# Kernel tuning notes

Measured on AMD Instinct MI355X. Metric: run time of the kernel, lower is better.

## Reference

```python
import jax, jax.numpy as jnp
import numpy as np

EPS = 1e-5  # torch LayerNorm default


def setup_inputs() -> dict:
    key = jax.random.key(0)
    ks = jax.random.split(key, 16)
    B, S, E = 2, 2048, 1024
    H, DK, DV = 16, 64, 64
    s_in = 1.0 / np.sqrt(E)
    s_ctx = 1.0 / np.sqrt(H * DV)
    return {
        "Q": jax.random.normal(ks[0], (B, S, E), jnp.float32),
        "K": jax.random.normal(ks[1], (B, S, E), jnp.float32),
        "V": jax.random.normal(ks[2], (B, S, E), jnp.float32),
        "attn_mask": jax.random.randint(ks[3], (B, S, S), 0, 2).astype(bool),
        "Wq": jax.random.normal(ks[4], (E, H * DK), jnp.float32) * s_in,
        "bq": jnp.zeros((H * DK,), jnp.float32),
        "Wk": jax.random.normal(ks[5], (E, H * DK), jnp.float32) * s_in,
        "bk": jnp.zeros((H * DK,), jnp.float32),
        "Wv": jax.random.normal(ks[6], (E, H * DV), jnp.float32) * s_in,
        "bv": jnp.zeros((H * DV,), jnp.float32),
        "Wo": jax.random.normal(ks[7], (H * DV, E), jnp.float32) * s_ctx,
        "bo": jnp.zeros((E,), jnp.float32),
        "gamma": jnp.ones((E,), jnp.float32),
        "beta": jnp.zeros((E,), jnp.float32),
        "n_heads": 16,
        "d_k": 64,
        "d_v": 64,
    }


def reference(Q, K, V, attn_mask, Wq, bq, Wk, bk, Wv, bv, Wo, bo, gamma, beta,
              n_heads, d_k, d_v):
    B, S, E = Q.shape
    # QKV projections -> [B, H, S, d]
    q = (Q @ Wq + bq).reshape(B, S, n_heads, d_k).transpose(0, 2, 1, 3)
    k = (K @ Wk + bk).reshape(B, S, n_heads, d_k).transpose(0, 2, 1, 3)
    v = (V @ Wv + bv).reshape(B, S, n_heads, d_v).transpose(0, 2, 1, 3)
    # scaled dot-product attention with explicit [B,H,S,S] scores
    scores = jnp.einsum('bhqd,bhkd->bhqk', q, k) / np.sqrt(d_k).astype(jnp.float32)
    scores = jnp.where(attn_mask[:, None, :, :], jnp.float32(-1e9), scores)
    attn = jax.nn.softmax(scores, axis=-1)
    context = jnp.einsum('bhqk,bhkd->bhqd', attn, v)
    context = context.transpose(0, 2, 1, 3).reshape(B, S, n_heads * d_v)
    output = context @ Wo + bo
    # residual + LayerNorm over last dim
    x = output + Q
    mu = jnp.mean(x, axis=-1, keepdims=True)
    var = jnp.mean(jnp.square(x - mu), axis=-1, keepdims=True)
    y = (x - mu) * jax.lax.rsqrt(var + EPS) * gamma + beta
    return (y, attn)
```

## Files before the change

### kernel.cpp

```cpp
#include <hip/hip_runtime.h>
#include <cstdint>
#include <cstddef>

#define Bc 2
#define Sc 2048
#define Ec 1024
#define Hc 16
#define Dc 64
#define BSc 4096
#define BHc 32

typedef __attribute__((ext_vector_type(8))) short bf16x8;
typedef __attribute__((ext_vector_type(4))) float f32x4;

__device__ __forceinline__ uint16_t f2b(float x) {
  union { float f; uint32_t u; } v; v.f = x;
  return (uint16_t)((v.u + 0x7FFFu + ((v.u >> 16) & 1u)) >> 16);
}

__global__ void conv_bf16(const float* __restrict__ src, uint16_t* __restrict__ dst, int n) {
  int i = (blockIdx.x * blockDim.x + threadIdx.x) * 4;
  if (i < n) {
    float4 v = *(const float4*)(src + i);
    ushort4 o;
    o.x = f2b(v.x); o.y = f2b(v.y); o.z = f2b(v.z); o.w = f2b(v.w);
    *(ushort4*)(dst + i) = o;
  }
}

__global__ void transpose_bf16(const float* __restrict__ src, uint16_t* __restrict__ dst) {
  __shared__ uint16_t tile[32][33];
  int x0 = blockIdx.x * 32, y0 = blockIdx.y * 32;
  int tx = threadIdx.x & 31, ty = threadIdx.x >> 5;
#pragma unroll
  for (int i = 0; i < 32; i += 8)
    tile[ty + i][tx] = f2b(src[(size_t)(y0 + ty + i) * 1024 + x0 + tx]);
  __syncthreads();
#pragma unroll
  for (int i = 0; i < 32; i += 8)
    dst[(size_t)(x0 + ty + i) * 1024 + y0 + tx] = tile[tx][ty + i];
}

__global__ __launch_bounds__(256) void gemm_proj(
    const uint16_t* __restrict__ A, const uint16_t* __restrict__ BT,
    const float* __restrict__ bias, uint16_t* __restrict__ out, int mode) {
  const int K = 1024;
  __shared__ uint16_t As[128 * 40];
  __shared__ uint16_t Bs[128 * 40];
  int n0 = blockIdx.x * 128, m0 = blockIdx.y * 128;
  int t = threadIdx.x;
  int wave = t >> 6, lane = t & 63;
  int wm = (wave >> 1) * 64, wn = (wave & 1) * 64;
  int quad = lane >> 4, l16 = lane & 15;

  f32x4 acc[4][4];
#pragma unroll
  for (int i = 0; i < 4; i++)
#pragma unroll
    for (int j = 0; j < 4; j++) acc[i][j] = (f32x4)(0.0f);

  int srow = t >> 1, scol = (t & 1) * 16;

  for (int k0 = 0; k0 < K; k0 += 32) {
    const uint16_t* ag = A + (size_t)(m0 + srow) * K + k0 + scol;
    const uint16_t* bg = BT + (size_t)(n0 + srow) * K + k0 + scol;
    uint4 av0 = *(const uint4*)ag;
    uint4 av1 = *(const uint4*)(ag + 8);
    uint4 bv0 = *(const uint4*)bg;
    uint4 bv1 = *(const uint4*)(bg + 8);
    __syncthreads();
    *(uint4*)(As + srow * 40 + scol) = av0;
    *(uint4*)(As + srow * 40 + scol + 8) = av1;
    *(uint4*)(Bs + srow * 40 + scol) = bv0;
    *(uint4*)(Bs + srow * 40 + scol + 8) = bv1;
    __syncthreads();
    bf16x8 af[4], bfr[4];
#pragma unroll
    for (int i = 0; i < 4; i++)
      af[i] = *(const bf16x8*)(As + (wm + i * 16 + l16) * 40 + quad * 8);
#pragma unroll
    for (int j = 0; j < 4; j++)
      bfr[j] = *(const bf16x8*)(Bs + (wn + j * 16 + l16) * 40 + quad * 8);
#pragma unroll
    for (int i = 0; i < 4; i++)
#pragma unroll
      for (int j = 0; j < 4; j++)
        acc[i][j] = __builtin_amdgcn_mfma_f32_16x16x32_bf16(af[i], bfr[j], acc[i][j], 0, 0, 0);
  }
#pragma unroll
  for (int i = 0; i < 4; i++)
#pragma unroll
    for (int j = 0; j < 4; j++) {
      int col = n0 + wn + j * 16 + l16;
      float bval = bias[col];
      int h = col >> 6, d = col & 63;
#pragma unroll
      for (int r = 0; r < 4; r++) {
        int row = m0 + wm + i * 16 + quad * 4 + r;
        int b = row >> 11, s = row & 2047;
        uint16_t hv = f2b(acc[i][j][r] + bval);
        if (mode == 0)
          out[(size_t)((b * Hc + h) * Sc + s) * Dc + d] = hv;
        else
          out[(size_t)((b * Hc + h) * Dc + d) * Sc + s] = hv;
      }
    }
}

__global__ __launch_bounds__(256) void gemm_out(
    const uint16_t* __restrict__ A, const uint16_t* __restrict__ BT,
    const float* __restrict__ bias, const float* __restrict__ resid,
    float* __restrict__ x) {
  const int K = 1024;
  __shared__ uint16_t As[128 * 40];
  __shared__ uint16_t Bs[128 * 40];
  int n0 = blockIdx.x * 128, m0 = blockIdx.y * 128;
  int t = threadIdx.x;
  int wave = t >> 6, lane = t & 63;
  int wm = (wave >> 1) * 64, wn = (wave & 1) * 64;
  int quad = lane >> 4, l16 = lane & 15;

  f32x4 acc[4][4];
#pragma unroll
  for (int i = 0; i < 4; i++)
#pragma unroll
    for (int j = 0; j < 4; j++) acc[i][j] = (f32x4)(0.0f);

  int srow = t >> 1, scol = (t & 1) * 16;
  for (int k0 = 0; k0 < K; k0 += 32) {
    const uint16_t* ag = A + (size_t)(m0 + srow) * K + k0 + scol;
    const uint16_t* bg = BT + (size_t)(n0 + srow) * K + k0 + scol;
    uint4 av0 = *(const uint4*)ag;
    uint4 av1 = *(const uint4*)(ag + 8);
    uint4 bv0 = *(const uint4*)bg;
    uint4 bv1 = *(const uint4*)(bg + 8);
    __syncthreads();
    *(uint4*)(As + srow * 40 + scol) = av0;
    *(uint4*)(As + srow * 40 + scol + 8) = av1;
    *(uint4*)(Bs + srow * 40 + scol) = bv0;
    *(uint4*)(Bs + srow * 40 + scol + 8) = bv1;
    __syncthreads();
    bf16x8 af[4], bfr[4];
#pragma unroll
    for (int i = 0; i < 4; i++)
      af[i] = *(const bf16x8*)(As + (wm + i * 16 + l16) * 40 + quad * 8);
#pragma unroll
    for (int j = 0; j < 4; j++)
      bfr[j] = *(const bf16x8*)(Bs + (wn + j * 16 + l16) * 40 + quad * 8);
#pragma unroll
    for (int i = 0; i < 4; i++)
#pragma unroll
      for (int j = 0; j < 4; j++)
        acc[i][j] = __builtin_amdgcn_mfma_f32_16x16x32_bf16(af[i], bfr[j], acc[i][j], 0, 0, 0);
  }
#pragma unroll
  for (int i = 0; i < 4; i++)
#pragma unroll
    for (int j = 0; j < 4; j++) {
      int col = n0 + wn + j * 16 + l16;
      float bval = bias[col];
#pragma unroll
      for (int r = 0; r < 4; r++) {
        int row = m0 + wm + i * 16 + quad * 4 + r;
        x[(size_t)row * 1024 + col] = acc[i][j][r] + bval + resid[(size_t)row * 1024 + col];
      }
    }
}

__global__ __launch_bounds__(256) void fused_attn(
    const uint16_t* __restrict__ qh,
    const uint16_t* __restrict__ kh,
    const uint16_t* __restrict__ vT,
    const int* __restrict__ mask,
    float* __restrict__ attn,
    uint16_t* __restrict__ ctx) {
  __shared__ uint16_t Qs[64 * 72];
  __shared__ uint16_t Ks[64 * 72];
  __shared__ uint16_t Vs[64 * 72];
  __shared__ uint16_t Ps[64 * 72];
  __shared__ float rinv_s[64];

  int m0 = blockIdx.x * 64;
  int bh = blockIdx.y;
  int b = bh >> 4;
  int t = threadIdx.x;
  int wave = t >> 6, lane = t & 63;
  int quad = lane >> 4, l16 = lane & 15;

  int srow = t >> 2, scol = (t & 3) * 16;

  {
    const uint16_t* qg = qh + (size_t)(bh * Sc + m0 + srow) * Dc + scol;
    uint4 q0 = *(const uint4*)qg;
    uint4 q1 = *(const uint4*)(qg + 8);
    *(uint4*)(Qs + srow * 72 + scol) = q0;
    *(uint4*)(Qs + srow * 72 + scol + 8) = q1;
  }
  __syncthreads();

  int m = m0 + wave * 16 + l16;
  const int* mrow = mask + (size_t)(b * Sc + m) * Sc;

  bf16x8 qf0 = *(const bf16x8*)(Qs + (wave * 16 + l16) * 72 + quad * 8);
  bf16x8 qf1 = *(const bf16x8*)(Qs + (wave * 16 + l16) * 72 + 32 + quad * 8);

  float rs = 0.0f;
  for (int k0 = 0; k0 < Sc; k0 += 64) {
    const uint16_t* kg = kh + (size_t)(bh * Sc + k0 + srow) * Dc + scol;
    uint4 kv0 = *(const uint4*)kg;
    uint4 kv1 = *(const uint4*)(kg + 8);
    __syncthreads();
    *(uint4*)(Ks + srow * 72 + scol) = kv0;
    *(uint4*)(Ks + srow * 72 + scol + 8) = kv1;
    __syncthreads();
    int4 mv[4];
#pragma unroll
    for (int j = 0; j < 4; j++)
      mv[j] = *(const int4*)(mrow + k0 + j * 16 + quad * 4);
    f32x4 sacc[4];
#pragma unroll
    for (int j = 0; j < 4; j++) sacc[j] = (f32x4)(0.0f);
#pragma unroll
    for (int j = 0; j < 4; j++) {
      bf16x8 kf0 = *(const bf16x8*)(Ks + (j * 16 + l16) * 72 + quad * 8);
      bf16x8 kf1 = *(const bf16x8*)(Ks + (j * 16 + l16) * 72 + 32 + quad * 8);
      sacc[j] = __builtin_amdgcn_mfma_f32_16x16x32_bf16(kf0, qf0, sacc[j], 0, 0, 0);
      sacc[j] = __builtin_amdgcn_mfma_f32_16x16x32_bf16(kf1, qf1, sacc[j], 0, 0, 0);
    }
#pragma unroll
    for (int j = 0; j < 4; j++) {
      rs += mv[j].x ? 0.0f : __expf(sacc[j][0] * 0.125f);
      rs += mv[j].y ? 0.0f : __expf(sacc[j][1] * 0.125f);
      rs += mv[j].z ? 0.0f : __expf(sacc[j][2] * 0.125f);
      rs += mv[j].w ? 0.0f : __expf(sacc[j][3] * 0.125f);
    }
  }
  rs += __shfl_xor(rs, 16);
  rs += __shfl_xor(rs, 32);
  if (lane < 16) rinv_s[wave * 16 + l16] = 1.0f / rs;
  __syncthreads();
  float rv = rinv_s[wave * 16 + l16];

  f32x4 cacc[4];
#pragma unroll
  for (int j = 0; j < 4; j++) cacc[j] = (f32x4)(0.0f);

  for (int k0 = 0; k0 < Sc; k0 += 64) {
    const uint16_t* kg = kh + (size_t)(bh * Sc + k0 + srow) * Dc + scol;
    const uint16_t* vg = vT + (size_t)(bh * Dc + srow) * Sc + k0 + scol;
    uint4 kv0 = *(const uint4*)kg;
    uint4 kv1 = *(const uint4*)(kg + 8);
    uint4 vv0 = *(const uint4*)vg;
    uint4 vv1 = *(const uint4*)(vg + 8);
    __syncthreads();
    *(uint4*)(Ks + srow * 72 + scol) = kv0;
    *(uint4*)(Ks + srow * 72 + scol + 8) = kv1;
    *(uint4*)(Vs + srow * 72 + scol) = vv0;
    *(uint4*)(Vs + srow * 72 + scol + 8) = vv1;
    __syncthreads();
    int4 mv[4];
#pragma unroll
    for (int j = 0; j < 4; j++)
      mv[j] = *(const int4*)(mrow + k0 + j * 16 + quad * 4);
    f32x4 sacc[4];
#pragma unroll
    for (int j = 0; j < 4; j++) sacc[j] = (f32x4)(0.0f);
#pragma unroll
    for (int j = 0; j < 4; j++) {
      bf16x8 kf0 = *(const bf16x8*)(Ks + (j * 16 + l16) * 72 + quad * 8);
      bf16x8 kf1 = *(const bf16x8*)(Ks + (j * 16 + l16) * 72 + 32 + quad * 8);
      sacc[j] = __builtin_amdgcn_mfma_f32_16x16x32_bf16(kf0, qf0, sacc[j], 0, 0, 0);
      sacc[j] = __builtin_amdgcn_mfma_f32_16x16x32_bf16(kf1, qf1, sacc[j], 0, 0, 0);
    }
    float* arow = attn + (size_t)(bh * Sc + m) * Sc + k0;
#pragma unroll
    for (int j = 0; j < 4; j++) {
      float p0 = mv[j].x ? 0.0f : __expf(sacc[j][0] * 0.125f) * rv;
      float p1 = mv[j].y ? 0.0f : __expf(sacc[j][1] * 0.125f) * rv;
      float p2 = mv[j].z ? 0.0f : __expf(sacc[j][2] * 0.125f) * rv;
      float p3 = mv[j].w ? 0.0f : __expf(sacc[j][3] * 0.125f) * rv;
      *(float4*)(arow + j * 16 + quad * 4) = make_float4(p0, p1, p2, p3);
      union { uint16_t u[4]; uint2 v; } pk;
      pk.u[0] = f2b(p0); pk.u[1] = f2b(p1); pk.u[2] = f2b(p2); pk.u[3] = f2b(p3);
      *(uint2*)(Ps + (wave * 16 + l16) * 72 + j * 16 + quad * 4) = pk.v;
    }
    bf16x8 pf0 = *(const bf16x8*)(Ps + (wave * 16 + l16) * 72 + quad * 8);
    bf16x8 pf1 = *(const bf16x8*)(Ps + (wave * 16 + l16) * 72 + 32 + quad * 8);
#pragma unroll
    for (int j = 0; j < 4; j++) {
      bf16x8 vf0 = *(const bf16x8*)(Vs + (j * 16 + l16) * 72 + quad * 8);
      bf16x8 vf1 = *(const bf16x8*)(Vs + (j * 16 + l16) * 72 + 32 + quad * 8);
      cacc[j] = __builtin_amdgcn_mfma_f32_16x16x32_bf16(pf0, vf0, cacc[j], 0, 0, 0);
      cacc[j] = __builtin_amdgcn_mfma_f32_16x16x32_bf16(pf1, vf1, cacc[j], 0, 0, 0);
    }
  }
  int h = bh & 15;
#pragma unroll
  for (int j = 0; j < 4; j++) {
    int d = j * 16 + l16;
#pragma unroll
    for (int r = 0; r < 4; r++) {
      int s = m0 + wave * 16 + quad * 4 + r;
      ctx[(size_t)(b * Sc + s) * (Hc * Dc) + h * Dc + d] = f2b(cacc[j][r]);
    }
  }
}

__global__ __launch_bounds__(256) void ln_kernel(
    const float* __restrict__ x, const float* __restrict__ gamma,
    const float* __restrict__ beta, float* __restrict__ y) {
  int row = blockIdx.x;
  int t = threadIdx.x;
  const float* xr = x + (size_t)row * 1024;
  float4 v = *(const float4*)(xr + t * 4);
  float s = v.x + v.y + v.z + v.w;
  float s2 = v.x * v.x + v.y * v.y + v.z * v.z + v.w * v.w;
#pragma unroll
  for (int o = 1; o < 64; o <<= 1) {
    s += __shfl_xor(s, o);
    s2 += __shfl_xor(s2, o);
  }
  __shared__ float ss[4], ss2[4];
  int wave = t >> 6, lane = t & 63;
  if (lane == 0) { ss[wave] = s; ss2[wave] = s2; }
  __syncthreads();
  s = ss[0] + ss[1] + ss[2] + ss[3];
  s2 = ss2[0] + ss2[1] + ss2[2] + ss2[3];
  float mu = s * (1.0f / 1024.0f);
  float var = s2 * (1.0f / 1024.0f) - mu * mu;
  float rstd = rsqrtf(var + 1e-5f);
  float4 g = *(const float4*)(gamma + t * 4);
  float4 be = *(const float4*)(beta + t * 4);
  float4 o;
  o.x = (v.x - mu) * rstd * g.x + be.x;
  o.y = (v.y - mu) * rstd * g.y + be.y;
  o.z = (v.z - mu) * rstd * g.z + be.z;
  o.w = (v.w - mu) * rstd * g.w + be.w;
  *(float4*)(y + (size_t)row * 1024 + t * 4) = o;
}

extern "C" void kernel_launch(void* const* d_in, const int* in_sizes, int n_in,
                              void* d_out, int out_size, void* d_ws, size_t ws_size,
                              hipStream_t stream) {
  const float* Q = (const float*)d_in[0];
  const float* K = (const float*)d_in[1];
  const float* V = (const float*)d_in[2];
  const int* mask = (const int*)d_in[3];
  const float* Wq = (const float*)d_in[4];
  const float* bq = (const float*)d_in[5];
  const float* Wk = (const float*)d_in[6];
  const float* bk = (const float*)d_in[7];
  const float* Wv = (const float*)d_in[8];
  const float* bv = (const float*)d_in[9];
  const float* Wo = (const float*)d_in[10];
  const float* bo = (const float*)d_in[11];
  const float* gamma = (const float*)d_in[12];
  const float* beta = (const float*)d_in[13];

  float* y = (float*)d_out;
  float* attn = (float*)d_out + (size_t)BSc * Ec;

  char* ws = (char*)d_ws;
  size_t off = 0;
  auto alloc = [&](size_t bytes) -> void* {
    void* p = ws + off;
    off = (off + bytes + 255) & ~(size_t)255;
    return p;
  };
  uint16_t* Qb  = (uint16_t*)alloc((size_t)BSc * Ec * 2);
  uint16_t* Kb  = (uint16_t*)alloc((size_t)BSc * Ec * 2);
  uint16_t* Vb  = (uint16_t*)alloc((size_t)BSc * Ec * 2);
  uint16_t* WqT = (uint16_t*)alloc((size_t)Ec * Ec * 2);
  uint16_t* WkT = (uint16_t*)alloc((size_t)Ec * Ec * 2);
  uint16_t* WvT = (uint16_t*)alloc((size_t)Ec * Ec * 2);
  uint16_t* WoT = (uint16_t*)alloc((size_t)Ec * Ec * 2);
  uint16_t* qh  = (uint16_t*)alloc((size_t)BHc * Sc * Dc * 2);
  uint16_t* kh  = (uint16_t*)alloc((size_t)BHc * Sc * Dc * 2);
  uint16_t* vT  = (uint16_t*)alloc((size_t)BHc * Dc * Sc * 2);
  uint16_t* ctx = (uint16_t*)alloc((size_t)BSc * Ec * 2);
  float* xres   = (float*)alloc((size_t)BSc * Ec * 4);

  const int n_qkv = BSc * Ec;

  conv_bf16<<<n_qkv / 1024, 256, 0, stream>>>(Q, Qb, n_qkv);
  conv_bf16<<<n_qkv / 1024, 256, 0, stream>>>(K, Kb, n_qkv);
  conv_bf16<<<n_qkv / 1024, 256, 0, stream>>>(V, Vb, n_qkv);
  dim3 tg(32, 32);
  transpose_bf16<<<tg, 256, 0, stream>>>(Wq, WqT);
  transpose_bf16<<<tg, 256, 0, stream>>>(Wk, WkT);
  transpose_bf16<<<tg, 256, 0, stream>>>(Wv, WvT);
  transpose_bf16<<<tg, 256, 0, stream>>>(Wo, WoT);
  dim3 pg(Ec / 128, BSc / 128);
  gemm_proj<<<pg, 256, 0, stream>>>(Qb, WqT, bq, qh, 0);
  gemm_proj<<<pg, 256, 0, stream>>>(Kb, WkT, bk, kh, 0);
  gemm_proj<<<pg, 256, 0, stream>>>(Vb, WvT, bv, vT, 1);
  dim3 fg(Sc / 64, BHc);
  fused_attn<<<fg, 256, 0, stream>>>(qh, kh, vT, mask, attn, ctx);
  gemm_out<<<pg, 256, 0, stream>>>(ctx, WoT, bo, Q, xres);
  ln_kernel<<<BSc, 256, 0, stream>>>(xres, gamma, beta, y);
}
```

Measured before the change: 1.022 ms.

## Bit-pack attention mask and drop LDS staging of Q/K/V in fused attention

Adds a pre-pass that packs the int32 mask into 64-bit ballot words, so each attention iteration reads one word per row instead of 64 ints. This cuts the mask traffic in the attention kernel, which is re-read by every head. The attention kernel also stops staging Q, K and V tiles through shared memory with block barriers. Each wave now loads its MFMA fragments straight from global memory and keeps only a per-wave P buffer, which removes the __syncthreads. In exchange, K and V are loaded redundantly by each of the 4 waves and rely on cache hits, and one extra kernel launch is added.

Result: slower. 1.143 ms (+11.8%).

```diff
diff --git a/kernel.cpp b/kernel.cpp
--- a/kernel.cpp
+++ b/kernel.cpp
@@ -39,6 +39,16 @@
 #pragma unroll
   for (int i = 0; i < 32; i += 8)
     dst[(size_t)(x0 + ty + i) * 1024 + y0 + tx] = tile[tx][ty + i];
+}
+
+__global__ void pack_mask(const int* __restrict__ mask, unsigned long long* __restrict__ pm, int n64) {
+  int idx = blockIdx.x * (blockDim.x >> 6) + (threadIdx.x >> 6);
+  int lane = threadIdx.x & 63;
+  if (idx < n64) {
+    int v = mask[(size_t)idx * 64 + lane];
+    unsigned long long b = __ballot(v != 0);
+    if (lane == 0) pm[idx] = b;
+  }
 }
 
 __global__ __launch_bounds__(256) void gemm_proj(
@@ -171,14 +181,10 @@
     const uint16_t* __restrict__ qh,
     const uint16_t* __restrict__ kh,
     const uint16_t* __restrict__ vT,
-    const int* __restrict__ mask,
+    const unsigned long long* __restrict__ pmask,
     float* __restrict__ attn,
     uint16_t* __restrict__ ctx) {
-  __shared__ uint16_t Qs[64 * 72];
-  __shared__ uint16_t Ks[64 * 72];
-  __shared__ uint16_t Vs[64 * 72];
-  __shared__ uint16_t Ps[64 * 72];
-  __shared__ float rinv_s[64];
+  __shared__ uint16_t Ps[4][16 * 72];
 
   int m0 = blockIdx.x * 64;
   int bh = blockIdx.y;
@@ -187,109 +193,82 @@
   int wave = t >> 6, lane = t & 63;
   int quad = lane >> 4, l16 = lane & 15;
 
-  int srow = t >> 2, scol = (t & 3) * 16;
-
-  {
-    const uint16_t* qg = qh + (size_t)(bh * Sc + m0 + srow) * Dc + scol;
-    uint4 q0 = *(const uint4*)qg;
-    uint4 q1 = *(const uint4*)(qg + 8);
-    *(uint4*)(Qs + srow * 72 + scol) = q0;
-    *(uint4*)(Qs + srow * 72 + scol + 8) = q1;
-  }
-  __syncthreads();
-
   int m = m0 + wave * 16 + l16;
-  const int* mrow = mask + (size_t)(b * Sc + m) * Sc;
-
-  bf16x8 qf0 = *(const bf16x8*)(Qs + (wave * 16 + l16) * 72 + quad * 8);
-  bf16x8 qf1 = *(const bf16x8*)(Qs + (wave * 16 + l16) * 72 + 32 + quad * 8);
+  const unsigned long long* pmr = pmask + (size_t)(b * Sc + m) * (Sc / 64);
+
+  const uint16_t* qg = qh + (size_t)(bh * Sc + m) * Dc;
+  bf16x8 qf0 = *(const bf16x8*)(qg + quad * 8);
+  bf16x8 qf1 = *(const bf16x8*)(qg + 32 + quad * 8);
+
+  const uint16_t* kbase = kh + (size_t)bh * Sc * Dc;
+  const uint16_t* vbase = vT + (size_t)bh * Dc * Sc;
 
   float rs = 0.0f;
   for (int k0 = 0; k0 < Sc; k0 += 64) {
-    const uint16_t* kg = kh + (size_t)(bh * Sc + k0 + srow) * Dc + scol;
-    uint4 kv0 = *(const uint4*)kg;
-    uint4 kv1 = *(const uint4*)(kg + 8);
-    __syncthreads();
-    *(uint4*)(Ks + srow * 72 + scol) = kv0;
-    *(uint4*)(Ks + srow * 72 + scol + 8) = kv1;
-    __syncthreads();
-    int4 mv[4];
-#pragma unroll
-    for (int j = 0; j < 4; j++)
-      mv[j] = *(const int4*)(mrow + k0 + j * 16 + quad * 4);
+    unsigned long long mk = pmr[k0 >> 6];
     f32x4 sacc[4];
 #pragma unroll
     for (int j = 0; j < 4; j++) sacc[j] = (f32x4)(0.0f);
 #pragma unroll
     for (int j = 0; j < 4; j++) {
-      bf16x8 kf0 = *(const bf16x8*)(Ks + (j * 16 + l16) * 72 + quad * 8);
-      bf16x8 kf1 = *(const bf16x8*)(Ks + (j * 16 + l16) * 72 + 32 + quad * 8);
+      const uint16_t* kg = kbase + (size_t)(k0 + j * 16 + l16) * Dc + quad * 8;
+      bf16x8 kf0 = *(const bf16x8*)kg;
+      bf16x8 kf1 = *(const bf16x8*)(kg + 32);
       sacc[j] = __builtin_amdgcn_mfma_f32_16x16x32_bf16(kf0, qf0, sacc[j], 0, 0, 0);
       sacc[j] = __builtin_amdgcn_mfma_f32_16x16x32_bf16(kf1, qf1, sacc[j], 0, 0, 0);
     }
 #pragma unroll
     for (int j = 0; j < 4; j++) {
-      rs += mv[j].x ? 0.0f : __expf(sacc[j][0] * 0.125f);
-      rs += mv[j].y ? 0.0f : __expf(sacc[j][1] * 0.125f);
-      rs += mv[j].z ? 0.0f : __expf(sacc[j][2] * 0.125f);
-      rs += mv[j].w ? 0.0f : __expf(sacc[j][3] * 0.125f);
+      int base = j * 16 + quad * 4;
+#pragma unroll
+      for (int r = 0; r < 4; r++) {
+        float e = __expf(sacc[j][r] * 0.125f);
+        rs += ((mk >> (base + r)) & 1ull) ? 0.0f : e;
+      }
     }
   }
   rs += __shfl_xor(rs, 16);
   rs += __shfl_xor(rs, 32);
-  if (lane < 16) rinv_s[wave * 16 + l16] = 1.0f / rs;
-  __syncthreads();
-  float rv = rinv_s[wave * 16 + l16];
+  float rv = 1.0f / rs;
 
   f32x4 cacc[4];
 #pragma unroll
   for (int j = 0; j < 4; j++) cacc[j] = (f32x4)(0.0f);
+  uint16_t* Pw = Ps[wave];
 
   for (int k0 = 0; k0 < Sc; k0 += 64) {
-    const uint16_t* kg = kh + (size_t)(bh * Sc + k0 + srow) * Dc + scol;
-    const uint16_t* vg = vT + (size_t)(bh * Dc + srow) * Sc + k0 + scol;
-    uint4 kv0 = *(const uint4*)kg;
-    uint4 kv1 = *(const uint4*)(kg + 8);
-    uint4 vv0 = *(const uint4*)vg;
-    uint4 vv1 = *(const uint4*)(vg + 8);
-    __syncthreads();
-    *(uint4*)(Ks + srow * 72 + scol) = kv0;
-    *(uint4*)(Ks + srow * 72 + scol + 8) = kv1;
-    *(uint4*)(Vs + srow * 72 + scol) = vv0;
-    *(uint4*)(Vs + srow * 72 + scol + 8) = vv1;
-    __syncthreads();
-    int4 mv[4];
-#pragma unroll
-    for (int j = 0; j < 4; j++)
-      mv[j] = *(const int4*)(mrow + k0 + j * 16 + quad * 4);
+    unsigned long long mk = pmr[k0 >> 6];
     f32x4 sacc[4];
 #pragma unroll
     for (int j = 0; j < 4; j++) sacc[j] = (f32x4)(0.0f);
 #pragma unroll
     for (int j = 0; j < 4; j++) {
-      bf16x8 kf0 = *(const bf16x8*)(Ks + (j * 16 + l16) * 72 + quad * 8);
-      bf16x8 kf1 = *(const bf16x8*)(Ks + (j * 16 + l16) * 72 + 32 + quad * 8);
+      const uint16_t* kg = kbase + (size_t)(k0 + j * 16 + l16) * Dc + quad * 8;
+      bf16x8 kf0 = *(const bf16x8*)kg;
+      bf16x8 kf1 = *(const bf16x8*)(kg + 32);
       sacc[j] = __builtin_amdgcn_mfma_f32_16x16x32_bf16(kf0, qf0, sacc[j], 0, 0, 0);
       sacc[j] = __builtin_amdgcn_mfma_f32_16x16x32_bf16(kf1, qf1, sacc[j], 0, 0, 0);
     }
     float* arow = attn + (size_t)(bh * Sc + m) * Sc + k0;
 #pragma unroll
     for (int j = 0; j < 4; j++) {
-      float p0 = mv[j].x ? 0.0f : __expf(sacc[j][0] * 0.125f) * rv;
-      float p1 = mv[j].y ? 0.0f : __expf(sacc[j][1] * 0.125f) * rv;
-      float p2 = mv[j].z ? 0.0f : __expf(sacc[j][2] * 0.125f) * rv;
-      float p3 = mv[j].w ? 0.0f : __expf(sacc[j][3] * 0.125f) * rv;
-      *(float4*)(arow + j * 16 + quad * 4) = make_float4(p0, p1, p2, p3);
+      int base = j * 16 + quad * 4;
+      float p0 = ((mk >> (base + 0)) & 1ull) ? 0.0f : __expf(sacc[j][0] * 0.125f) * rv;
+      float p1 = ((mk >> (base + 1)) & 1ull) ? 0.0f : __expf(sacc[j][1] * 0.125f) * rv;
+      float p2 = ((mk >> (base + 2)) & 1ull) ? 0.0f : __expf(sacc[j][2] * 0.125f) * rv;
+      float p3 = ((mk >> (base + 3)) & 1ull) ? 0.0f : __expf(sacc[j][3] * 0.125f) * rv;
+      *(float4*)(arow + base) = make_float4(p0, p1, p2, p3);
       union { uint16_t u[4]; uint2 v; } pk;
       pk.u[0] = f2b(p0); pk.u[1] = f2b(p1); pk.u[2] = f2b(p2); pk.u[3] = f2b(p3);
-      *(uint2*)(Ps + (wave * 16 + l16) * 72 + j * 16 + quad * 4) = pk.v;
-    }
-    bf16x8 pf0 = *(const bf16x8*)(Ps + (wave * 16 + l16) * 72 + quad * 8);
-    bf16x8 pf1 = *(const bf16x8*)(Ps + (wave * 16 + l16) * 72 + 32 + quad * 8);
-#pragma unroll
-    for (int j = 0; j < 4; j++) {
-      bf16x8 vf0 = *(const bf16x8*)(Vs + (j * 16 + l16) * 72 + quad * 8);
-      bf16x8 vf1 = *(const bf16x8*)(Vs + (j * 16 + l16) * 72 + 32 + quad * 8);
+      *(uint2*)(Pw + l16 * 72 + base) = pk.v;
+    }
+    bf16x8 pf0 = *(const bf16x8*)(Pw + l16 * 72 + quad * 8);
+    bf16x8 pf1 = *(const bf16x8*)(Pw + l16 * 72 + 32 + quad * 8);
+#pragma unroll
+    for (int j = 0; j < 4; j++) {
+      const uint16_t* vg = vbase + (size_t)(j * 16 + l16) * Sc + k0 + quad * 8;
+      bf16x8 vf0 = *(const bf16x8*)vg;
+      bf16x8 vf1 = *(const bf16x8*)(vg + 32);
       cacc[j] = __builtin_amdgcn_mfma_f32_16x16x32_bf16(pf0, vf0, cacc[j], 0, 0, 0);
       cacc[j] = __builtin_amdgcn_mfma_f32_16x16x32_bf16(pf1, vf1, cacc[j], 0, 0, 0);
     }
@@ -379,12 +358,15 @@
   uint16_t* vT  = (uint16_t*)alloc((size_t)BHc * Dc * Sc * 2);
   uint16_t* ctx = (uint16_t*)alloc((size_t)BSc * Ec * 2);
   float* xres   = (float*)alloc((size_t)BSc * Ec * 4);
+  unsigned long long* pm = (unsigned long long*)alloc((size_t)Bc * Sc * (Sc / 64) * 8);
 
   const int n_qkv = BSc * Ec;
+  const int n64 = Bc * Sc * (Sc / 64);
 
   conv_bf16<<<n_qkv / 1024, 256, 0, stream>>>(Q, Qb, n_qkv);
   conv_bf16<<<n_qkv / 1024, 256, 0, stream>>>(K, Kb, n_qkv);
   conv_bf16<<<n_qkv / 1024, 256, 0, stream>>>(V, Vb, n_qkv);
+  pack_mask<<<n64 / 4, 256, 0, stream>>>(mask, pm, n64);
   dim3 tg(32, 32);
   transpose_bf16<<<tg, 256, 0, stream>>>(Wq, WqT);
   transpose_bf16<<<tg, 256, 0, stream>>>(Wk, WkT);
@@ -395,7 +377,7 @@
   gemm_proj<<<pg, 256, 0, stream>>>(Kb, WkT, bk, kh, 0);
   gemm_proj<<<pg, 256, 0, stream>>>(Vb, WvT, bv, vT, 1);
   dim3 fg(Sc / 64, BHc);
-  fused_attn<<<fg, 256, 0, stream>>>(qh, kh, vT, mask, attn, ctx);
+  fused_attn<<<fg, 256, 0, stream>>>(qh, kh, vT, pm, attn, ctx);
   gemm_out<<<pg, 256, 0, stream>>>(ctx, WoT, bo, Q, xres);
   ln_kernel<<<BSc, 256, 0, stream>>>(xres, gamma, beta, y);
 }
```
